# Optimization experiments

Hardware: AMD Instinct MI355X
Metric: run time of the kernel (lower is better)

The kernel has to match this reference:

```python
import jax, jax.numpy as jnp
import numpy as np

MODEL_DIM = 4096
NH = 32          # query heads
NG = 8           # kv heads (query groups)
HD = MODEL_DIM // NH   # 128, == kv_head_dim in the module
KV_DIM = NG * HD       # 1024
BASE = 50000.0
B, S = 1, 2048


def setup_inputs() -> dict:
    key = jax.random.key(0)
    ks = jax.random.split(key, 3)
    s = 0.02
    return {
        "x": jax.random.normal(ks[0], (B, S, MODEL_DIM), jnp.float32),
        "Wqkv": jax.random.normal(ks[1], (MODEL_DIM, MODEL_DIM + 2 * KV_DIM), jnp.float32) * s,
        "bqkv": jnp.zeros((MODEL_DIM + 2 * KV_DIM,), jnp.float32),
        "Wo": jax.random.normal(ks[2], (MODEL_DIM, MODEL_DIM), jnp.float32) * s,
        "bo": jnp.zeros((MODEL_DIM,), jnp.float32),
    }


def _rope_tables(seq_len):
    # Llama-style RoPE: inv_freq over even dims, emb = concat(freqs, freqs)
    inv_freq = 1.0 / (BASE ** (jnp.arange(0, HD, 2, dtype=jnp.float32) / HD))
    t = jnp.arange(seq_len, dtype=jnp.float32)  # offset = 0 (no cache)
    freqs = t[:, None] * inv_freq[None, :]      # [S, HD/2]
    emb = jnp.concatenate([freqs, freqs], axis=-1)  # [S, HD]
    return jnp.cos(emb), jnp.sin(emb)


def _rotate_half(x):
    x1, x2 = jnp.split(x, 2, axis=-1)
    return jnp.concatenate([-x2, x1], axis=-1)


def reference(x, Wqkv, bqkv, Wo, bo):
    Bsz, Sl, _ = x.shape
    fused = x @ Wqkv + bqkv                                   # [B, S, D + 2*KV]
    q, k, v = jnp.split(fused, [MODEL_DIM, MODEL_DIM + KV_DIM], axis=-1)
    q = q.reshape(Bsz, Sl, NH, HD).transpose(0, 2, 1, 3)      # [B, NH, S, HD]
    k = k.reshape(Bsz, Sl, NG, HD).transpose(0, 2, 1, 3)      # [B, NG, S, HD]
    v = v.reshape(Bsz, Sl, NG, HD).transpose(0, 2, 1, 3)

    cos, sin = _rope_tables(Sl)                               # [S, HD] each
    q = q * cos + _rotate_half(q) * sin
    k = k * cos + _rotate_half(k) * sin

    # GQA without duplicating KV: group query heads per shared KV head
    G = NH // NG
    qg = q.reshape(Bsz, NG, G, Sl, HD)                        # [B, NG, G, S, HD]
    scale = 1.0 / jnp.sqrt(jnp.asarray(HD, q.dtype))
    scores = jnp.einsum('bngsd,bntd->bngst', qg, k) * scale   # [B, NG, G, S, S]
    causal = jnp.tril(jnp.ones((Sl, Sl), dtype=bool))
    scores = jnp.where(causal, scores, jnp.finfo(scores.dtype).min)
    attn = jax.nn.softmax(scores, axis=-1)
    out = jnp.einsum('bngst,bntd->bngsd', attn, v)            # [B, NG, G, S, HD]
    out = out.reshape(Bsz, NH, Sl, HD).transpose(0, 2, 1, 3).reshape(Bsz, Sl, MODEL_DIM)
    return out @ Wo + bo
```

## Files before the change

kernel.cpp:

```cpp
#include <hip/hip_runtime.h>
#include <hip/hip_bf16.h>
#include <math.h>

#define S_LEN  2048
#define MDIM   4096
#define NHEADS 32
#define NKV    8
#define HD     128
#define KVDIM  1024
#define NFUSED (MDIM + 2 * KVDIM)

typedef short bf16x8 __attribute__((ext_vector_type(8)));
typedef float f32x4 __attribute__((ext_vector_type(4)));

__device__ __forceinline__ unsigned short f2b(float f) {
  union { float f; unsigned int u; } v; v.f = f;
  unsigned int r = v.u + 0x7FFFu + ((v.u >> 16) & 1u);
  return (unsigned short)(r >> 16);
}
__device__ __forceinline__ float b2f(unsigned short h) {
  union { unsigned int u; float f; } v; v.u = ((unsigned int)h) << 16;
  return v.f;
}

__device__ __forceinline__ void async_copy16(const void* g, void* l) {
  __builtin_amdgcn_global_load_lds(
      (const __attribute__((address_space(1))) unsigned int*)g,
      (__attribute__((address_space(3))) unsigned int*)l, 16, 0, 0);
}

__global__ __launch_bounds__(256) void convert_x(
    const float* __restrict__ src, unsigned short* __restrict__ dst) {
  size_t i = (size_t)blockIdx.x * 256 + threadIdx.x;
  const float4 a = ((const float4*)src)[2 * i];
  const float4 b = ((const float4*)src)[2 * i + 1];
  unsigned short o[8] = {f2b(a.x), f2b(a.y), f2b(a.z), f2b(a.w),
                         f2b(b.x), f2b(b.y), f2b(b.z), f2b(b.w)};
  *(int4*)(dst + 8 * i) = *(const int4*)o;
}

__global__ __launch_bounds__(256) void transpose_convert(
    const float* __restrict__ W, unsigned short* __restrict__ WT, int K,
    int N) {
  __shared__ unsigned short t[64 * 72];
  const int k0 = blockIdx.y << 6, n0 = blockIdx.x << 6;
  const int tid = threadIdx.x;
#pragma unroll
  for (int it = 0; it < 4; ++it) {
    int idx = it * 256 + tid;
    int r = idx & 63;
    int c = ((idx >> 6) & 15) << 2;
    const float4 v = *(const float4*)(W + (size_t)(k0 + r) * N + n0 + c);
    t[(c + 0) * 72 + r] = f2b(v.x);
    t[(c + 1) * 72 + r] = f2b(v.y);
    t[(c + 2) * 72 + r] = f2b(v.z);
    t[(c + 3) * 72 + r] = f2b(v.w);
  }
  __syncthreads();
  const int n = tid >> 2, kk = (tid & 3) << 4;
  *(int4*)(WT + (size_t)(n0 + n) * K + k0 + kk) = *(int4*)&t[n * 72 + kk];
  *(int4*)(WT + (size_t)(n0 + n) * K + k0 + kk + 8) =
      *(int4*)&t[n * 72 + kk + 8];
}

__global__ __launch_bounds__(512, 2) void gemm1_kernel(
    const unsigned short* __restrict__ xb,
    const unsigned short* __restrict__ WT, const float* __restrict__ bias,
    unsigned short* __restrict__ Qb, unsigned short* __restrict__ Kb,
    unsigned short* __restrict__ Vt) {
  __shared__ unsigned short sm[2][32768];

  const int tid = threadIdx.x;
  const int bn = blockIdx.x, bm = blockIdx.y;
  const int lane = tid & 63, wave = tid >> 6;
  const int lrow = lane & 15, quad = lane >> 4;
  const int wrow = wave >> 2, wcol = wave & 3;

  f32x4 acc[8][4];
#pragma unroll
  for (int i = 0; i < 8; ++i)
#pragma unroll
    for (int j = 0; j < 4; ++j) {
      f32x4 z = {0.f, 0.f, 0.f, 0.f};
      acc[i][j] = z;
    }

  const int lr8 = lane >> 3, lc8 = lane & 7;
  const int baser = wave * 8 + lr8;
  const size_t swz = (size_t)((lc8 ^ (baser & 7)) << 3);
  const unsigned short* sA = xb + (size_t)(bm * 256 + baser) * MDIM + swz;
  const unsigned short* sB = WT + (size_t)(bn * 256 + baser) * MDIM + swz;

  auto stage = [&](int slot, int k0) {
#pragma unroll
    for (int c = 0; c < 4; ++c) {
      unsigned short* dA = &sm[slot][(c * 64 + wave * 8) * 64];
      unsigned short* dB = &sm[slot][16384 + (c * 64 + wave * 8) * 64];
      async_copy16(sA + (size_t)c * 64 * MDIM + k0, dA);
      async_copy16(sB + (size_t)c * 64 * MDIM + k0, dB);
    }
  };

  const int arow = wrow * 128 + lrow;
  const int brow = wcol * 64 + lrow;
  const int co0 = (quad ^ (lrow & 7)) << 3;
  const int co1 = ((4 + quad) ^ (lrow & 7)) << 3;

  stage(0, 0);

  for (int kt = 0; kt < 64; ++kt) {
    const int p = kt & 1;
    asm volatile("s_waitcnt vmcnt(0)" ::: "memory");
    __builtin_amdgcn_s_barrier();
    __builtin_amdgcn_sched_barrier(0);

    if (kt < 63) stage(p ^ 1, (kt + 1) << 6);

    const unsigned short* Asl = &sm[p][0];
    const unsigned short* Bsl = &sm[p][16384];
    __builtin_amdgcn_s_setprio(1);
#pragma unroll
    for (int kk = 0; kk < 2; ++kk) {
      const int co = kk ? co1 : co0;
      bf16x8 bfr[4];
#pragma unroll
      for (int j = 0; j < 4; ++j)
        bfr[j] = *(const bf16x8*)&Bsl[(brow + j * 16) * 64 + co];
#pragma unroll
      for (int i = 0; i < 8; ++i) {
        bf16x8 af = *(const bf16x8*)&Asl[(arow + i * 16) * 64 + co];
#pragma unroll
        for (int j = 0; j < 4; ++j)
          acc[i][j] = __builtin_amdgcn_mfma_f32_16x16x32_bf16(
              af, bfr[j], acc[i][j], 0, 0, 0);
      }
    }
    __builtin_amdgcn_s_setprio(0);
  }
  __syncthreads();

  unsigned short* Ct = &sm[0][0];
#pragma unroll 1
  for (int h = 0; h < 2; ++h) {
    const int slot = 2 * bn + h;
    if ((wcol >> 1) == h) {
#pragma unroll
      for (int i = 0; i < 8; ++i)
#pragma unroll
        for (int j = 0; j < 4; ++j) {
          int lc = (wcol & 1) * 64 + j * 16 + lrow;
          float bv = bias[slot * 128 + lc];
#pragma unroll
          for (int r = 0; r < 4; ++r) {
            int lrw = wrow * 128 + i * 16 + quad * 4 + r;
            Ct[lrw * 132 + lc] = f2b(acc[i][j][r] + bv);
          }
        }
    }
    __syncthreads();

    if (slot < 40) {
#pragma unroll 4
      for (int it = 0; it < 32; ++it) {
        int row = it * 8 + wave;
        int d = lane;
        float x1 = b2f(Ct[row * 132 + d]);
        float x2 = b2f(Ct[row * 132 + d + 64]);
        int s = bm * 256 + row;
        float inv_freq = __expf(-0.16905903569f * (float)d);
        float ang = (float)s * inv_freq;
        float c = cosf(ang), sn = sinf(ang);
        float o1 = x1 * c - x2 * sn;
        float o2 = x2 * c + x1 * sn;
        unsigned short* dst;
        if (slot < 32)
          dst = Qb + ((size_t)slot * S_LEN + s) * HD;
        else
          dst = Kb + ((size_t)(slot - 32) * S_LEN + s) * HD;
        dst[d] = f2b(o1);
        dst[d + 64] = f2b(o2);
      }
    } else {
      const int g = slot - 40;
      unsigned short* Vtg = Vt + (size_t)g * HD * S_LEN;
      const int dp = tid >> 3;
      const int sq = (tid & 7) << 5;
      unsigned short buf0[32], buf1[32];
#pragma unroll
      for (int i = 0; i < 32; ++i) {
        unsigned int w = *(const unsigned int*)&Ct[(sq + i) * 132 + 2 * dp];
        buf0[i] = (unsigned short)(w & 0xffffu);
        buf1[i] = (unsigned short)(w >> 16);
      }
      const int s0 = bm * 256 + sq;
#pragma unroll
      for (int c = 0; c < 2; ++c) {
        unsigned short* dst = Vtg + (size_t)(2 * dp + c) * S_LEN + s0;
        const unsigned short* b = c ? buf1 : buf0;
#pragma unroll
        for (int q4 = 0; q4 < 4; ++q4)
          *(int4*)(dst + q4 * 8) = *(const int4*)(b + q4 * 8);
      }
    }
    __syncthreads();
  }
}

__global__ __launch_bounds__(256, 4) void gemm2_kernel(
    const unsigned short* __restrict__ Ab16,
    const unsigned short* __restrict__ BT, const float* __restrict__ bias,
    float* __restrict__ C) {
  __shared__ unsigned short As[128 * 32];
  __shared__ unsigned short Bs[128 * 32];

  const int tid = threadIdx.x;
  const int bn = blockIdx.x, bm = blockIdx.y;
  const int lane = tid & 63, wave = tid >> 6;
  const int lrow = lane & 15, quad = lane >> 4;
  const int wr = (wave & 1) * 64, wc = (wave >> 1) * 64;

  f32x4 acc[4][4];
#pragma unroll
  for (int i = 0; i < 4; ++i)
#pragma unroll
    for (int j = 0; j < 4; ++j) {
      f32x4 z = {0.f, 0.f, 0.f, 0.f};
      acc[i][j] = z;
    }

  const unsigned short* gA = Ab16 +
      (size_t)(bm * 128 + wave * 32 + (lane >> 2)) * MDIM + ((lane & 3) << 3);
  const unsigned short* gB = BT +
      (size_t)(bn * 128 + wave * 32 + (lane >> 2)) * MDIM + ((lane & 3) << 3);
  unsigned short* lA = As + wave * 32 * 32;
  unsigned short* lB = Bs + wave * 32 * 32;

  for (int k0 = 0; k0 < MDIM; k0 += 32) {
    async_copy16(gA + k0, lA);
    async_copy16(gA + k0 + (size_t)16 * MDIM, lA + 16 * 32);
    async_copy16(gB + k0, lB);
    async_copy16(gB + k0 + (size_t)16 * MDIM, lB + 16 * 32);
    __syncthreads();
    bf16x8 af[4], bfr[4];
#pragma unroll
    for (int i = 0; i < 4; ++i)
      af[i] = *(const bf16x8*)&As[(wr + 16 * i + lrow) * 32 + 8 * quad];
#pragma unroll
    for (int j = 0; j < 4; ++j)
      bfr[j] = *(const bf16x8*)&Bs[(wc + 16 * j + lrow) * 32 + 8 * quad];
#pragma unroll
    for (int i = 0; i < 4; ++i)
#pragma unroll
      for (int j = 0; j < 4; ++j)
        acc[i][j] = __builtin_amdgcn_mfma_f32_16x16x32_bf16(af[i], bfr[j],
                                                            acc[i][j], 0, 0, 0);
    __syncthreads();
  }

#pragma unroll
  for (int i = 0; i < 4; ++i)
#pragma unroll
    for (int j = 0; j < 4; ++j) {
      int gcol = bn * 128 + wc + 16 * j + lrow;
      float bv = bias[gcol];
#pragma unroll
      for (int r = 0; r < 4; ++r) {
        int grow = bm * 128 + wr + 16 * i + 4 * quad + r;
        C[(size_t)grow * MDIM + gcol] = acc[i][j][r] + bv;
      }
    }
}

__device__ __forceinline__ void stage_kv(const unsigned short* __restrict__ Kg,
                                         const unsigned short* __restrict__ Vg,
                                         int jtile, unsigned short* KsBuf,
                                         unsigned short* VsBuf, int wv,
                                         int lane) {
  const unsigned short* kg = Kg + (size_t)jtile * 64 * HD;
  const unsigned short* vg = Vg + jtile * 64;
#pragma unroll
  for (int it = 0; it < 4; ++it) {
    int kr = wv * 16 + it * 4 + (lane >> 4);
    async_copy16(kg + (size_t)kr * HD + (((lane & 15) ^ (kr & 7)) << 3),
                 KsBuf + (wv * 16 + it * 4) * 128);
    int vr = wv * 32 + it * 8 + (lane >> 3);
    async_copy16(vg + (size_t)vr * S_LEN + (((lane & 7) ^ (vr & 7)) << 3),
                 VsBuf + (wv * 32 + it * 8) * 64);
  }
}

__global__ __launch_bounds__(256, 2) void flash_kernel(
    const unsigned short* __restrict__ Qb, const unsigned short* __restrict__ Kb,
    const unsigned short* __restrict__ Vt, unsigned short* __restrict__ attnb) {
  __shared__ __align__(16) unsigned short Ks[2][64 * 128];
  __shared__ __align__(16) unsigned short Vs[2][128 * 64];
  __shared__ __align__(16) unsigned short Ps[64 * 72];

  const int tid = threadIdx.x;
  const int bid = blockIdx.x;
  const int h = bid & 31;
  const int qt = 31 - (bid >> 5);
  const int g = h >> 2;
  const int wv = tid >> 6, lane = tid & 63;
  const int lrow = lane & 15, quad = lane >> 4;
  const float scale = 0.08838834764831845f;

  const unsigned short* Qg = Qb + ((size_t)h * S_LEN + qt * 64) * HD;
  bf16x8 qf[4];
#pragma unroll
  for (int ks = 0; ks < 4; ++ks)
    qf[ks] = *(const bf16x8*)(Qg + (size_t)(wv * 16 + lrow) * HD + ks * 32 +
                              quad * 8);

  bf16x8 ones;
#pragma unroll
  for (int i = 0; i < 8; ++i) ones[i] = (short)0x3F80;

  const unsigned short* Kg = Kb + (size_t)g * S_LEN * HD;
  const unsigned short* Vg = Vt + (size_t)g * HD * S_LEN;

  f32x4 l_acc = {0.f, 0.f, 0.f, 0.f};
  f32x4 o_acc[8];
#pragma unroll
  for (int jc = 0; jc < 8; ++jc) {
    f32x4 z = {0.f, 0.f, 0.f, 0.f};
    o_acc[jc] = z;
  }

  stage_kv(Kg, Vg, 0, &Ks[0][0], &Vs[0][0], wv, lane);

  for (int jt = 0; jt <= qt; ++jt) {
    const int cb = jt & 1;
    asm volatile("s_waitcnt vmcnt(0)" ::: "memory");
    __builtin_amdgcn_s_barrier();
    __builtin_amdgcn_sched_barrier(0);

    if (jt < qt)
      stage_kv(Kg, Vg, jt + 1, &Ks[cb ^ 1][0], &Vs[cb ^ 1][0], wv, lane);

    f32x4 s_acc[4];
#pragma unroll
    for (int j = 0; j < 4; ++j) {
      f32x4 z = {0.f, 0.f, 0.f, 0.f};
      s_acc[j] = z;
    }
#pragma unroll
    for (int ks = 0; ks < 4; ++ks)
#pragma unroll
      for (int j = 0; j < 4; ++j) {
        int row = j * 16 + lrow;
        bf16x8 bk = *(const bf16x8*)&Ks[cb][row * 128 +
                                           (((ks * 4 + quad) ^ (row & 7)) << 3)];
        s_acc[j] = __builtin_amdgcn_mfma_f32_16x16x32_bf16(qf[ks], bk,
                                                           s_acc[j], 0, 0, 0);
      }

    if (jt == qt) {
#pragma unroll
      for (int r = 0; r < 4; ++r) {
        int grow = qt * 64 + wv * 16 + quad * 4 + r;
#pragma unroll
        for (int j = 0; j < 4; ++j) {
          int gcol = jt * 64 + j * 16 + lrow;
          float p =
              (gcol <= grow) ? __expf(s_acc[j][r] * scale - 12.0f) : 0.f;
          Ps[(wv * 16 + quad * 4 + r) * 72 + j * 16 + lrow] = f2b(p);
        }
      }
    } else {
#pragma unroll
      for (int r = 0; r < 4; ++r)
#pragma unroll
        for (int j = 0; j < 4; ++j) {
          float p = __expf(s_acc[j][r] * scale - 12.0f);
          Ps[(wv * 16 + quad * 4 + r) * 72 + j * 16 + lrow] = f2b(p);
        }
    }
    asm volatile("s_waitcnt lgkmcnt(0)" ::: "memory");
    __builtin_amdgcn_sched_barrier(0);

#pragma unroll
    for (int kk = 0; kk < 2; ++kk) {
      bf16x8 ap =
          *(const bf16x8*)&Ps[(wv * 16 + lrow) * 72 + kk * 32 + 8 * quad];
      l_acc = __builtin_amdgcn_mfma_f32_16x16x32_bf16(ap, ones, l_acc, 0, 0, 0);
#pragma unroll
      for (int jc = 0; jc < 8; ++jc) {
        int row = jc * 16 + lrow;
        bf16x8 bv = *(const bf16x8*)&Vs[cb][row * 64 +
                                            (((kk * 4 + quad) ^ (row & 7)) << 3)];
        o_acc[jc] = __builtin_amdgcn_mfma_f32_16x16x32_bf16(ap, bv, o_acc[jc],
                                                            0, 0, 0);
      }
    }
    __builtin_amdgcn_s_barrier();
  }

#pragma unroll
  for (int r = 0; r < 4; ++r) {
    float inv_l = 1.0f / l_acc[r];
    int row = qt * 64 + wv * 16 + quad * 4 + r;
#pragma unroll
    for (int jc = 0; jc < 8; ++jc) {
      int col = jc * 16 + lrow;
      attnb[(size_t)row * MDIM + h * HD + col] = f2b(o_acc[jc][r] * inv_l);
    }
  }
}

extern "C" void kernel_launch(void* const* d_in, const int* in_sizes, int n_in,
                              void* d_out, int out_size, void* d_ws,
                              size_t ws_size, hipStream_t stream) {
  const float* x = (const float*)d_in[0];
  const float* Wqkv = (const float*)d_in[1];
  const float* bqkv = (const float*)d_in[2];
  const float* Wo = (const float*)d_in[3];
  const float* bo = (const float*)d_in[4];
  float* out = (float*)d_out;

  unsigned char* ws = (unsigned char*)d_ws;
  unsigned short* WT = (unsigned short*)ws;
  unsigned short* WoT = (unsigned short*)ws;
  unsigned short* attnb = (unsigned short*)(ws + 33554432);
  unsigned short* Qb = (unsigned short*)(ws + 50331648);
  unsigned short* Kb = (unsigned short*)(ws + 67108864);
  unsigned short* Vt = (unsigned short*)(ws + 71303168);
  unsigned short* xb = (unsigned short*)d_out;

  convert_x<<<(S_LEN * MDIM / 8) / 256, 256, 0, stream>>>(x, xb);
  transpose_convert<<<dim3(NFUSED / 64, MDIM / 64), 256, 0, stream>>>(
      Wqkv, WT, MDIM, NFUSED);
  gemm1_kernel<<<dim3(NFUSED / 256, S_LEN / 256), 512, 0, stream>>>(
      xb, WT, bqkv, Qb, Kb, Vt);
  transpose_convert<<<dim3(MDIM / 64, MDIM / 64), 256, 0, stream>>>(Wo, WoT,
                                                                    MDIM, MDIM);
  flash_kernel<<<S_LEN / 64 * NHEADS, 256, 0, stream>>>(Qb, Kb, Vt, attnb);
  gemm2_kernel<<<dim3(MDIM / 128, S_LEN / 128), 256, 0, stream>>>(attnb, WoT,
                                                                  bo, out);
}
```

Baseline: 503.2 us.

## Interleave async prefetch with MFMA phases in gemm1; retile gemm2 to 128x256 double-buffered

In gemm1, the next K-tile's global-to-LDS copies are split into four chunks, each issued between LDS fragment loads and MFMA groups and separated by barriers, so memory traffic overlaps compute instead of being issued all at once. gemm2 is rewritten from a single-buffered 128x128 tile with 256 threads and K-step 32 into a 512-thread, 128x256 tile with K-step 64. It uses a double-buffered, XOR-swizzled LDS layout and the same phased prefetch and priority scheme. The trade-offs are more LDS and register pressure per block, fewer gemm2 blocks, and extra barriers per iteration.

Measured after the change: 500.7 us. No clear change (-0.5%).

```diff
diff --git a/kernel.cpp b/kernel.cpp
--- a/kernel.cpp
+++ b/kernel.cpp
@@ -91,14 +91,17 @@
   const unsigned short* sA = xb + (size_t)(bm * 256 + baser) * MDIM + swz;
   const unsigned short* sB = WT + (size_t)(bn * 256 + baser) * MDIM + swz;
 
-  auto stage = [&](int slot, int k0) {
-#pragma unroll
-    for (int c = 0; c < 4; ++c) {
-      unsigned short* dA = &sm[slot][(c * 64 + wave * 8) * 64];
-      unsigned short* dB = &sm[slot][16384 + (c * 64 + wave * 8) * 64];
-      async_copy16(sA + (size_t)c * 64 * MDIM + k0, dA);
-      async_copy16(sB + (size_t)c * 64 * MDIM + k0, dB);
-    }
+  auto stageA2 = [&](int slot, int k0, int c0) {
+#pragma unroll
+    for (int c = c0; c < c0 + 2; ++c)
+      async_copy16(sA + (size_t)c * 64 * MDIM + k0,
+                   &sm[slot][(c * 64 + wave * 8) * 64]);
+  };
+  auto stageB2 = [&](int slot, int k0, int c0) {
+#pragma unroll
+    for (int c = c0; c < c0 + 2; ++c)
+      async_copy16(sB + (size_t)c * 64 * MDIM + k0,
+                   &sm[slot][16384 + (c * 64 + wave * 8) * 64]);
   };
 
   const int arow = wrow * 128 + lrow;
@@ -106,35 +109,95 @@
   const int co0 = (quad ^ (lrow & 7)) << 3;
   const int co1 = ((4 + quad) ^ (lrow & 7)) << 3;
 
-  stage(0, 0);
-
+  stageA2(0, 0, 0);
+  stageA2(0, 0, 2);
+  stageB2(0, 0, 0);
+  stageB2(0, 0, 2);
+
+#pragma unroll 1
   for (int kt = 0; kt < 64; ++kt) {
     const int p = kt & 1;
     asm volatile("s_waitcnt vmcnt(0)" ::: "memory");
     __builtin_amdgcn_s_barrier();
     __builtin_amdgcn_sched_barrier(0);
 
-    if (kt < 63) stage(p ^ 1, (kt + 1) << 6);
-
     const unsigned short* Asl = &sm[p][0];
     const unsigned short* Bsl = &sm[p][16384];
+    const int kn0 = (kt + 1) << 6;
+    const bool pref = kt < 63;
+    bf16x8 bfr[4], af[4];
+
+#pragma unroll
+    for (int j = 0; j < 4; ++j)
+      bfr[j] = *(const bf16x8*)&Bsl[(brow + j * 16) * 64 + co0];
+#pragma unroll
+    for (int i = 0; i < 4; ++i)
+      af[i] = *(const bf16x8*)&Asl[(arow + i * 16) * 64 + co0];
+    if (pref) stageA2(p ^ 1, kn0, 0);
+    __builtin_amdgcn_s_barrier();
+    asm volatile("s_waitcnt lgkmcnt(0)" ::: "memory");
+    __builtin_amdgcn_sched_barrier(0);
     __builtin_amdgcn_s_setprio(1);
 #pragma unroll
-    for (int kk = 0; kk < 2; ++kk) {
-      const int co = kk ? co1 : co0;
-      bf16x8 bfr[4];
+    for (int i = 0; i < 4; ++i)
 #pragma unroll
       for (int j = 0; j < 4; ++j)
-        bfr[j] = *(const bf16x8*)&Bsl[(brow + j * 16) * 64 + co];
-#pragma unroll
-      for (int i = 0; i < 8; ++i) {
-        bf16x8 af = *(const bf16x8*)&Asl[(arow + i * 16) * 64 + co];
-#pragma unroll
-        for (int j = 0; j < 4; ++j)
-          acc[i][j] = __builtin_amdgcn_mfma_f32_16x16x32_bf16(
-              af, bfr[j], acc[i][j], 0, 0, 0);
-      }
-    }
+        acc[i][j] = __builtin_amdgcn_mfma_f32_16x16x32_bf16(af[i], bfr[j],
+                                                            acc[i][j], 0, 0, 0);
+    __builtin_amdgcn_s_setprio(0);
+    __builtin_amdgcn_s_barrier();
+
+#pragma unroll
+    for (int i = 0; i < 4; ++i)
+      af[i] = *(const bf16x8*)&Asl[(arow + (4 + i) * 16) * 64 + co0];
+    if (pref) stageA2(p ^ 1, kn0, 2);
+    __builtin_amdgcn_s_barrier();
+    asm volatile("s_waitcnt lgkmcnt(0)" ::: "memory");
+    __builtin_amdgcn_sched_barrier(0);
+    __builtin_amdgcn_s_setprio(1);
+#pragma unroll
+    for (int i = 0; i < 4; ++i)
+#pragma unroll
+      for (int j = 0; j < 4; ++j)
+        acc[4 + i][j] = __builtin_amdgcn_mfma_f32_16x16x32_bf16(
+            af[i], bfr[j], acc[4 + i][j], 0, 0, 0);
+    __builtin_amdgcn_s_setprio(0);
+    __builtin_amdgcn_s_barrier();
+
+#pragma unroll
+    for (int j = 0; j < 4; ++j)
+      bfr[j] = *(const bf16x8*)&Bsl[(brow + j * 16) * 64 + co1];
+#pragma unroll
+    for (int i = 0; i < 4; ++i)
+      af[i] = *(const bf16x8*)&Asl[(arow + i * 16) * 64 + co1];
+    if (pref) stageB2(p ^ 1, kn0, 0);
+    __builtin_amdgcn_s_barrier();
+    asm volatile("s_waitcnt lgkmcnt(0)" ::: "memory");
+    __builtin_amdgcn_sched_barrier(0);
+    __builtin_amdgcn_s_setprio(1);
+#pragma unroll
+    for (int i = 0; i < 4; ++i)
+#pragma unroll
+      for (int j = 0; j < 4; ++j)
+        acc[i][j] = __builtin_amdgcn_mfma_f32_16x16x32_bf16(af[i], bfr[j],
+                                                            acc[i][j], 0, 0, 0);
+    __builtin_amdgcn_s_setprio(0);
+    __builtin_amdgcn_s_barrier();
+
+#pragma unroll
+    for (int i = 0; i < 4; ++i)
+      af[i] = *(const bf16x8*)&Asl[(arow + (4 + i) * 16) * 64 + co1];
+    if (pref) stageB2(p ^ 1, kn0, 2);
+    __builtin_amdgcn_s_barrier();
+    asm volatile("s_waitcnt lgkmcnt(0)" ::: "memory");
+    __builtin_amdgcn_sched_barrier(0);
+    __builtin_amdgcn_s_setprio(1);
+#pragma unroll
+    for (int i = 0; i < 4; ++i)
+#pragma unroll
+      for (int j = 0; j < 4; ++j)
+        acc[4 + i][j] = __builtin_amdgcn_mfma_f32_16x16x32_bf16(
+            af[i], bfr[j], acc[4 + i][j], 0, 0, 0);
     __builtin_amdgcn_s_setprio(0);
   }
   __syncthreads();
@@ -206,18 +269,17 @@
   }
 }
 
-__global__ __launch_bounds__(256, 4) void gemm2_kernel(
+__global__ __launch_bounds__(512, 2) void gemm2_kernel(
     const unsigned short* __restrict__ Ab16,
     const unsigned short* __restrict__ BT, const float* __restrict__ bias,
     float* __restrict__ C) {
-  __shared__ unsigned short As[128 * 32];
-  __shared__ unsigned short Bs[128 * 32];
+  __shared__ unsigned short sm[2][24576];
 
   const int tid = threadIdx.x;
   const int bn = blockIdx.x, bm = blockIdx.y;
   const int lane = tid & 63, wave = tid >> 6;
   const int lrow = lane & 15, quad = lane >> 4;
-  const int wr = (wave & 1) * 64, wc = (wave >> 1) * 64;
+  const int wrow = wave >> 2, wcol = wave & 3;
 
   f32x4 acc[4][4];
 #pragma unroll
@@ -228,44 +290,103 @@
       acc[i][j] = z;
     }
 
-  const unsigned short* gA = Ab16 +
-      (size_t)(bm * 128 + wave * 32 + (lane >> 2)) * MDIM + ((lane & 3) << 3);
-  const unsigned short* gB = BT +
-      (size_t)(bn * 128 + wave * 32 + (lane >> 2)) * MDIM + ((lane & 3) << 3);
-  unsigned short* lA = As + wave * 32 * 32;
-  unsigned short* lB = Bs + wave * 32 * 32;
-
-  for (int k0 = 0; k0 < MDIM; k0 += 32) {
-    async_copy16(gA + k0, lA);
-    async_copy16(gA + k0 + (size_t)16 * MDIM, lA + 16 * 32);
-    async_copy16(gB + k0, lB);
-    async_copy16(gB + k0 + (size_t)16 * MDIM, lB + 16 * 32);
-    __syncthreads();
-    bf16x8 af[4], bfr[4];
-#pragma unroll
-    for (int i = 0; i < 4; ++i)
-      af[i] = *(const bf16x8*)&As[(wr + 16 * i + lrow) * 32 + 8 * quad];
+  const int lr8 = lane >> 3, lc8 = lane & 7;
+  const int baser = wave * 8 + lr8;
+  const size_t swz = (size_t)((lc8 ^ (baser & 7)) << 3);
+  const unsigned short* sA = Ab16 + (size_t)(bm * 128 + baser) * MDIM + swz;
+  const unsigned short* sB = BT + (size_t)(bn * 256 + baser) * MDIM + swz;
+
+  auto stageA2 = [&](int slot, int k0) {
+#pragma unroll
+    for (int c = 0; c < 2; ++c)
+      async_copy16(sA + (size_t)c * 64 * MDIM + k0,
+                   &sm[slot][(c * 64 + wave * 8) * 64]);
+  };
+  auto stageB1 = [&](int slot, int k0, int c) {
+    async_copy16(sB + (size_t)c * 64 * MDIM + k0,
+                 &sm[slot][8192 + (c * 64 + wave * 8) * 64]);
+  };
+
+  const int arow = wrow * 64 + lrow;
+  const int brow = wcol * 64 + lrow;
+  const int co0 = (quad ^ (lrow & 7)) << 3;
+  const int co1 = ((4 + quad) ^ (lrow & 7)) << 3;
+
+  stageA2(0, 0);
+  stageB1(0, 0, 0);
+  stageB1(0, 0, 1);
+  stageB1(0, 0, 2);
+  stageB1(0, 0, 3);
+
+#pragma unroll 1
+  for (int kt = 0; kt < 64; ++kt) {
+    const int p = kt & 1;
+    asm volatile("s_waitcnt vmcnt(0)" ::: "memory");
+    __builtin_amdgcn_s_barrier();
+    __builtin_amdgcn_sched_barrier(0);
+
+    const unsigned short* Asl = &sm[p][0];
+    const unsigned short* Bsl = &sm[p][8192];
+    const int kn0 = (kt + 1) << 6;
+    const bool pref = kt < 63;
+    bf16x8 bfr[4], af[4];
+
 #pragma unroll
     for (int j = 0; j < 4; ++j)
-      bfr[j] = *(const bf16x8*)&Bs[(wc + 16 * j + lrow) * 32 + 8 * quad];
+      bfr[j] = *(const bf16x8*)&Bsl[(brow + j * 16) * 64 + co0];
+#pragma unroll
+    for (int i = 0; i < 4; ++i)
+      af[i] = *(const bf16x8*)&Asl[(arow + i * 16) * 64 + co0];
+    if (pref) {
+      stageA2(p ^ 1, kn0);
+      stageB1(p ^ 1, kn0, 0);
+    }
+    __builtin_amdgcn_s_barrier();
+    asm volatile("s_waitcnt lgkmcnt(0)" ::: "memory");
+    __builtin_amdgcn_sched_barrier(0);
+    __builtin_amdgcn_s_setprio(1);
 #pragma unroll
     for (int i = 0; i < 4; ++i)
 #pragma unroll
       for (int j = 0; j < 4; ++j)
         acc[i][j] = __builtin_amdgcn_mfma_f32_16x16x32_bf16(af[i], bfr[j],
                                                             acc[i][j], 0, 0, 0);
-    __syncthreads();
+    __builtin_amdgcn_s_setprio(0);
+    __builtin_amdgcn_s_barrier();
+
+#pragma unroll
+    for (int j = 0; j < 4; ++j)
+      bfr[j] = *(const bf16x8*)&Bsl[(brow + j * 16) * 64 + co1];
+#pragma unroll
+    for (int i = 0; i < 4; ++i)
+      af[i] = *(const bf16x8*)&Asl[(arow + i * 16) * 64 + co1];
+    if (pref) {
+      stageB1(p ^ 1, kn0, 1);
+      stageB1(p ^ 1, kn0, 2);
+      stageB1(p ^ 1, kn0, 3);
+    }
+    __builtin_amdgcn_s_barrier();
+    asm volatile("s_waitcnt lgkmcnt(0)" ::: "memory");
+    __builtin_amdgcn_sched_barrier(0);
+    __builtin_amdgcn_s_setprio(1);
+#pragma unroll
+    for (int i = 0; i < 4; ++i)
+#pragma unroll
+      for (int j = 0; j < 4; ++j)
+        acc[i][j] = __builtin_amdgcn_mfma_f32_16x16x32_bf16(af[i], bfr[j],
+                                                            acc[i][j], 0, 0, 0);
+    __builtin_amdgcn_s_setprio(0);
   }
 
 #pragma unroll
   for (int i = 0; i < 4; ++i)
 #pragma unroll
     for (int j = 0; j < 4; ++j) {
-      int gcol = bn * 128 + wc + 16 * j + lrow;
+      int gcol = bn * 256 + wcol * 64 + j * 16 + lrow;
       float bv = bias[gcol];
 #pragma unroll
       for (int r = 0; r < 4; ++r) {
-        int grow = bm * 128 + wr + 16 * i + 4 * quad + r;
+        int grow = bm * 128 + wrow * 64 + i * 16 + quad * 4 + r;
         C[(size_t)grow * MDIM + gcol] = acc[i][j][r] + bv;
       }
     }
@@ -435,6 +556,6 @@
   transpose_convert<<<dim3(MDIM / 64, MDIM / 64), 256, 0, stream>>>(Wo, WoT,
                                                                     MDIM, MDIM);
   flash_kernel<<<S_LEN / 64 * NHEADS, 256, 0, stream>>>(Qb, Kb, Vt, attnb);
-  gemm2_kernel<<<dim3(MDIM / 128, S_LEN / 128), 256, 0, stream>>>(attnb, WoT,
+  gemm2_kernel<<<dim3(MDIM / 256, S_LEN / 128), 512, 0, stream>>>(attnb, WoT,
                                                                   bo, out);
 }
```
